# Performance work log

Measured on AMD Instinct MI355X. Metric: run time of the kernel, lower is better.

The kernel has to match this reference:

```python
import jax, jax.numpy as jnp
import numpy as np

K_TOP = 2
N_HEADS = 4

def _ln(x, g, b, eps=1e-5):
    mu = x.mean(-1, keepdims=True)
    var = ((x - mu) ** 2).mean(-1, keepdims=True)
    return (x - mu) * jax.lax.rsqrt(var + eps) * g + b

def setup_inputs() -> dict:
    key = jax.random.key(0)
    ks = jax.random.split(key, 12)
    B, Na, dz, da = 1024, 32, 96, 32
    D = dz + da
    E, F, Hh, nr = 8, 1024, 512, 4
    s = 0.02
    rn = lambda k, sh: jax.random.normal(k, sh, jnp.float32) * s
    return dict(
        z=jax.random.normal(ks[0], (B, Na, dz), jnp.float32),
        a=jax.random.normal(ks[1], (B, Na, da), jnp.float32),
        w_gate=rn(ks[2], (Na * D, E)),
        w_in=rn(ks[3], (E, 3 * D, D)), b_in=jnp.zeros((E, 3 * D), jnp.float32),
        w_out=rn(ks[4], (E, D, D)), b_out=jnp.zeros((E, D), jnp.float32),
        ln1_g=jnp.ones((E, D), jnp.float32), ln1_b=jnp.zeros((E, D), jnp.float32),
        w1=rn(ks[5], (E, F, D)), b1=jnp.zeros((E, F), jnp.float32),
        w2=rn(ks[6], (E, D, F)), b2=jnp.zeros((E, D), jnp.float32),
        ln2_g=jnp.ones((E, D), jnp.float32), ln2_b=jnp.zeros((E, D), jnp.float32),
        head_w1=rn(ks[7], (Hh, Na * D)), head_b1=jnp.zeros((Hh,), jnp.float32),
        head_w2=rn(ks[8], (nr, Hh)), head_b2=jnp.zeros((nr,), jnp.float32),
    )

def reference(z, a, w_gate, w_in, b_in, w_out, b_out, ln1_g, ln1_b, w1, b1, w2, b2, ln2_g, ln2_b, head_w1, head_b1, head_w2, head_b2):
    B, Na, _ = z.shape
    x = jnp.concatenate([z, a], axis=-1)          # [B, Na, D]
    D = x.shape[-1]
    E = w_gate.shape[1]
    hd = D // N_HEADS
    x_flat = x.reshape(B, -1)                     # [B, Na*D]

    # --- NoisyTopKRouter (eval: clean logits only) ---
    logits = x_flat @ w_gate                      # [B, E]
    top_vals, top_idx = jax.lax.top_k(logits, min(K_TOP + 1, E))
    tk_gates = jax.nn.softmax(top_vals[:, :K_TOP], axis=1)
    gates = jnp.zeros_like(logits).at[jnp.arange(B)[:, None], top_idx[:, :K_TOP]].set(tk_gates)
    load = (gates > 0).sum(0).astype(jnp.float32)
    importance = gates.sum(0)
    cv2 = lambda v: jnp.var(v, ddof=1) / (jnp.mean(v) ** 2 + 1e-10)
    loss_bal = cv2(importance) + cv2(load) + jax.scipy.special.logsumexp(logits, axis=-1).mean()

    # --- expert (self-attn + FFN, pre/post-LN residual) ---
    def expert(p):
        wi, bi, wo, bo, g1, be1, W1, B1, W2, B2, g2, be2 = p
        qkv = x @ wi.T + bi                       # [B, Na, 3D]
        q, k_, v = jnp.split(qkv, 3, axis=-1)
        q = q.reshape(B, Na, N_HEADS, hd)
        k_ = k_.reshape(B, Na, N_HEADS, hd)
        v = v.reshape(B, Na, N_HEADS, hd)
        sc = jnp.einsum('bqhd,bkhd->bhqk', q, k_) / jnp.sqrt(jnp.float32(hd))
        att = jax.nn.softmax(sc, axis=-1)
        o = jnp.einsum('bhqk,bkhd->bqhd', att, v).reshape(B, Na, D)
        o = o @ wo.T + bo
        h = _ln(x + o, g1, be1)
        f = jax.nn.relu(h @ W1.T + B1) @ W2.T + B2
        return _ln(h + f, g2, be2)

    def body(y, p):
        *ep, gate_e = p                           # gate_e: [B]
        y = y + gate_e[:, None, None] * expert(tuple(ep))
        return y, None

    xs = (w_in, b_in, w_out, b_out, ln1_g, ln1_b, w1, b1, w2, b2, ln2_g, ln2_b, gates.T)
    y, _ = jax.lax.scan(body, jnp.zeros_like(x), xs)

    y_flat = y.reshape(B, -1)
    r = jax.nn.relu(y_flat @ head_w1.T + head_b1) @ head_w2.T + head_b2  # [B, n_r]
    return r, gates, loss_bal
```

## Files before the change

kernel.cpp:

```cpp
#include <hip/hip_runtime.h>
#include <math.h>


typedef short bf16x8 __attribute__((ext_vector_type(8)));
typedef float f32x4 __attribute__((ext_vector_type(4)));
typedef unsigned short u16;

#define MFMA(a, b, c) __builtin_amdgcn_mfma_f32_16x16x32_bf16((a), (b), (c), 0, 0, 0)

__device__ __forceinline__ u16 f2bf(float f) {
    unsigned int u = __float_as_uint(f);
    unsigned int r = u + 0x7FFFu + ((u >> 16) & 1u);
    return (u16)(r >> 16);
}
__device__ __forceinline__ float bf2f(u16 s) {
    return __uint_as_float(((unsigned int)s) << 16);
}

__global__ __launch_bounds__(256) void convert_kernel(
    const float* __restrict__ wi, const float* __restrict__ wo,
    const float* __restrict__ w1, const float* __restrict__ w2,
    const float* __restrict__ hw1,
    u16* __restrict__ wiB, u16* __restrict__ woB, u16* __restrict__ w1B,
    u16* __restrict__ w2B, u16* __restrict__ hw1B)
{
    int i4 = blockIdx.x * 256 + threadIdx.x;
    int e = i4 * 4;
    const float* s; u16* d; int off;
    if (e < 393216)       { s = wi;  d = wiB;  off = e; }
    else if (e < 524288)  { s = wo;  d = woB;  off = e - 393216; }
    else if (e < 1572864) { s = w1;  d = w1B;  off = e - 524288; }
    else if (e < 2621440) { s = w2;  d = w2B;  off = e - 1572864; }
    else                  { s = hw1; d = hw1B; off = e - 2621440; }
    float4 v = *(const float4*)(s + off);
    ushort4 o;
    o.x = f2bf(v.x); o.y = f2bf(v.y); o.z = f2bf(v.z); o.w = f2bf(v.w);
    *(ushort4*)(d + off) = o;
}

__global__ __launch_bounds__(256) void router_kernel(
    const float* __restrict__ z, const float* __restrict__ a,
    const float* __restrict__ wg,
    float* __restrict__ gates_out, float* __restrict__ lse_ws,
    int* __restrict__ topi, float* __restrict__ topg)
{
    __shared__ float red[256][9];
    const int b = blockIdx.x, t = threadIdx.x;
    float acc[8];
#pragma unroll
    for (int e = 0; e < 8; ++e) acc[e] = 0.f;
#pragma unroll
    for (int i = 0; i < 16; ++i) {
        int f = i * 256 + t;
        int n = f >> 7, d = f & 127;
        float xv = (d < 96) ? z[(b * 32 + n) * 96 + d]
                            : a[(b * 32 + n) * 32 + d - 96];
        const float* wr = wg + f * 8;
#pragma unroll
        for (int e = 0; e < 8; ++e) acc[e] += xv * wr[e];
    }
#pragma unroll
    for (int e = 0; e < 8; ++e) red[t][e] = acc[e];
    __syncthreads();
    for (int s = 128; s; s >>= 1) {
        if (t < s) {
#pragma unroll
            for (int e = 0; e < 8; ++e) red[t][e] += red[t + s][e];
        }
        __syncthreads();
    }
    if (t == 0) {
        float L[8];
#pragma unroll
        for (int e = 0; e < 8; ++e) L[e] = red[0][e];
        int i0 = 0;
#pragma unroll
        for (int e = 1; e < 8; ++e) if (L[e] > L[i0]) i0 = e;
        int i1 = -1; float v1 = -3.0e38f;
#pragma unroll
        for (int e = 0; e < 8; ++e) if (e != i0 && L[e] > v1) { v1 = L[e]; i1 = e; }
        float e1 = expf(v1 - L[i0]);
        float inv = 1.f / (1.f + e1);
        float g0 = inv, g1 = e1 * inv;
#pragma unroll
        for (int e = 0; e < 8; ++e)
            gates_out[b * 8 + e] = (e == i0) ? g0 : ((e == i1) ? g1 : 0.f);
        float m = L[i0];
        float se = 0.f;
#pragma unroll
        for (int e = 0; e < 8; ++e) se += expf(L[e] - m);
        lse_ws[b] = m + logf(se);
        topi[b * 2 + 0] = i0; topi[b * 2 + 1] = i1;
        topg[b * 2 + 0] = g0; topg[b * 2 + 1] = g1;
    }
}

__global__ __launch_bounds__(1024) void build_loss_kernel(
    const int* __restrict__ topi, const float* __restrict__ topg,
    const float* __restrict__ lse,
    int* __restrict__ cnts, int* __restrict__ ent, float* __restrict__ out_loss)
{
    __shared__ int sc_[8];
    __shared__ float red[9][1024];
    const int t = threadIdx.x;
    if (t < 8) sc_[t] = 0;
    __syncthreads();
    int e0 = topi[t * 2], e1 = topi[t * 2 + 1];
    float g0 = topg[t * 2], g1 = topg[t * 2 + 1];
    int p0 = atomicAdd(&sc_[e0], 1);
    ent[e0 * 2048 + p0] = t * 2;
    int p1 = atomicAdd(&sc_[e1], 1);
    ent[e1 * 2048 + p1] = t * 2 + 1;
#pragma unroll
    for (int e = 0; e < 8; ++e)
        red[e][t] = ((e == e0) ? g0 : 0.f) + ((e == e1) ? g1 : 0.f);
    red[8][t] = lse[t];
    __syncthreads();
    for (int s = 512; s; s >>= 1) {
        if (t < s) {
#pragma unroll
            for (int q = 0; q < 9; ++q) red[q][t] += red[q][t + s];
        }
        __syncthreads();
    }
    if (t == 0) {
        float cvv[2];
        for (int p = 0; p < 2; ++p) {
            float v[8], sum = 0.f;
            for (int e = 0; e < 8; ++e) {
                v[e] = p ? (float)sc_[e] : red[e][0];
                sum += v[e];
            }
            float mean = sum * (1.f / 8.f);
            float var = 0.f;
            for (int e = 0; e < 8; ++e) { float d = v[e] - mean; var += d * d; }
            var *= (1.f / 7.f);
            cvv[p] = var / (mean * mean + 1e-10f);
        }
        out_loss[0] = cvv[0] + cvv[1] + red[8][0] * (1.f / 1024.f);
    }
    __syncthreads();
    if (t < 8) cnts[t] = sc_[t];
}

#define SM_X 0
#define SM_Q 16384
#define SM_K 32768
#define SM_V 49152
#define SM_TOT 65536
#define PS_OFF 0
#define PQ_OFF 1024
#define MU_OFF 2048
#define RS_OFF 2304
#define ATTN_GRID 8192

__device__ __forceinline__ int tsw(int row, int col) {
    return row * 256 + ((col * 2) ^ ((row & 7) << 4));
}
__device__ __forceinline__ int vsw(int row, int col) {
    return row * 128 + ((col * 2) ^ ((row & 7) << 4));
}
__device__ __forceinline__ int fsw(int row, int col) {
    return row * 2048 + ((col * 2) ^ ((row & 7) << 4));
}

__global__ __launch_bounds__(512, 2) void attn_kernel(
    const float* __restrict__ z, const float* __restrict__ a,
    const u16* __restrict__ wiBF, const float* __restrict__ b_in,
    const u16* __restrict__ woBF, const float* __restrict__ b_out,
    const float* __restrict__ ln1g, const float* __restrict__ ln1b,
    const int* __restrict__ cnts, const int* __restrict__ ent,
    u16* __restrict__ h1g)
{
    const int e = blockIdx.x & 7, j = blockIdx.x >> 3;
    const int cnt = cnts[e];
    if (j * 2 >= cnt) return;
    const int base = j * 2;

    __shared__ __align__(16) char sm[SM_TOT];
    const int t = threadIdx.x;
    const int w = t >> 6, l = t & 63, l16 = l & 15, lk = l >> 4;
    const int ke = lk * 8;
    const int wr = w >> 2, wc = w & 3;
    const f32x4 zv = {0.f, 0.f, 0.f, 0.f};

    int bs[2];
#pragma unroll
    for (int i = 0; i < 2; ++i) {
        int gi = base + i;
        int idx = (gi < cnt) ? gi : (cnt - 1);
        bs[i] = ent[e * 2048 + idx];
    }

#pragma unroll
    for (int i = 0; i < 2; ++i) {
        int cid = i * 512 + t;
        int row = cid >> 4;
        int cb = (cid & 15) * 8;
        int b_ = bs[row >> 5] >> 1;
        int n = row & 31;
        float4 p0, p1;
        if (cb < 96) {
            const float* zp = z + ((size_t)b_ * 32 + n) * 96 + cb;
            p0 = *(const float4*)zp; p1 = *(const float4*)(zp + 4);
        } else {
            const float* ap = a + ((size_t)b_ * 32 + n) * 32 + (cb - 96);
            p0 = *(const float4*)ap; p1 = *(const float4*)(ap + 4);
        }
        bf16x8 pk;
        pk[0] = (short)f2bf(p0.x); pk[1] = (short)f2bf(p0.y);
        pk[2] = (short)f2bf(p0.z); pk[3] = (short)f2bf(p0.w);
        pk[4] = (short)f2bf(p1.x); pk[5] = (short)f2bf(p1.y);
        pk[6] = (short)f2bf(p1.z); pk[7] = (short)f2bf(p1.w);
        *(bf16x8*)(sm + SM_X + tsw(row, cb)) = pk;
    }
    __syncthreads();

    {
        f32x4 acc[2][6];
#pragma unroll
        for (int mt = 0; mt < 2; ++mt)
#pragma unroll
            for (int q = 0; q < 6; ++q) acc[mt][q] = zv;
#pragma unroll
        for (int ks = 0; ks < 4; ++ks) {
            bf16x8 af[2];
#pragma unroll
            for (int mt = 0; mt < 2; ++mt) {
                int R = wr * 32 + mt * 16 + l16;
                af[mt] = *(const bf16x8*)(sm + SM_X + tsw(R, ks * 32 + ke));
            }
#pragma unroll
            for (int q = 0; q < 6; ++q) {
                int jj = wc * 96 + q * 16 + l16;
                bf16x8 bb = *(const bf16x8*)(wiBF + e * 49152 + jj * 128 + ks * 32 + ke);
#pragma unroll
                for (int mt = 0; mt < 2; ++mt) acc[mt][q] = MFMA(af[mt], bb, acc[mt][q]);
            }
        }
#pragma unroll
        for (int q = 0; q < 6; ++q) {
            int C = wc * 96 + q * 16 + l16;
            float bj = b_in[e * 384 + C];
#pragma unroll
            for (int mt = 0; mt < 2; ++mt)
#pragma unroll
                for (int i = 0; i < 4; ++i) {
                    int R = wr * 32 + mt * 16 + lk * 4 + i;
                    u16 val = f2bf(acc[mt][q][i] + bj);
                    if (C < 128) {
                        *(u16*)(sm + SM_Q + tsw(R, C)) = val;
                    } else if (C < 256) {
                        *(u16*)(sm + SM_K + tsw(R, C - 128)) = val;
                    } else {
                        *(u16*)(sm + SM_V + vsw(C - 256, R)) = val;
                    }
                }
        }
    }
    __syncthreads();

    {
        const int tok = w >> 2, hb = (w & 3) * 32;
        const float scale = 0.17677669529663687f;
        bf16x8 qa[2], kf[2];
#pragma unroll
        for (int mt = 0; mt < 2; ++mt) {
            int R = tok * 32 + mt * 16 + l16;
            qa[mt] = *(const bf16x8*)(sm + SM_Q + tsw(R, hb + ke));
            kf[mt] = *(const bf16x8*)(sm + SM_K + tsw(R, hb + ke));
        }
        f32x4 sc[2][2];
        sc[0][0] = MFMA(qa[0], kf[0], zv); sc[0][1] = MFMA(qa[0], kf[1], zv);
        sc[1][0] = MFMA(qa[1], kf[0], zv); sc[1][1] = MFMA(qa[1], kf[1], zv);
#pragma unroll
        for (int mt = 0; mt < 2; ++mt)
#pragma unroll
            for (int i = 0; i < 4; ++i) {
                float v0 = sc[mt][0][i] * scale, v1 = sc[mt][1][i] * scale;
                float m = fmaxf(v0, v1);
                m = fmaxf(m, __shfl_xor(m, 1)); m = fmaxf(m, __shfl_xor(m, 2));
                m = fmaxf(m, __shfl_xor(m, 4)); m = fmaxf(m, __shfl_xor(m, 8));
                float e0 = __expf(v0 - m), e1 = __expf(v1 - m);
                float ssum = e0 + e1;
                ssum += __shfl_xor(ssum, 1); ssum += __shfl_xor(ssum, 2);
                ssum += __shfl_xor(ssum, 4); ssum += __shfl_xor(ssum, 8);
                float inv = 1.f / ssum;
                int row = mt * 16 + lk * 4 + i;
                char* pb = sm + SM_X + w * 2048 + row * 64;
                int sw = (row & 3) << 4;
                *(u16*)(pb + ((l16 * 2) ^ sw)) = f2bf(e0 * inv);
                *(u16*)(pb + (((16 + l16) * 2) ^ sw)) = f2bf(e1 * inv);
            }
        bf16x8 pa[2];
#pragma unroll
        for (int mt = 0; mt < 2; ++mt) {
            int row = mt * 16 + l16;
            pa[mt] = *(const bf16x8*)(sm + SM_X + w * 2048 + row * 64 +
                                      ((ke * 2) ^ ((row & 3) << 4)));
        }
        f32x4 o[2][2];
#pragma unroll
        for (int nt = 0; nt < 2; ++nt) {
            int rv = hb + nt * 16 + l16;
            bf16x8 vb = *(const bf16x8*)(sm + SM_V + vsw(rv, tok * 32 + ke));
            o[0][nt] = MFMA(pa[0], vb, zv);
            o[1][nt] = MFMA(pa[1], vb, zv);
        }
#pragma unroll
        for (int mt = 0; mt < 2; ++mt)
#pragma unroll
            for (int nt = 0; nt < 2; ++nt)
#pragma unroll
                for (int i = 0; i < 4; ++i) {
                    int R = tok * 32 + mt * 16 + lk * 4 + i;
                    int C = hb + nt * 16 + l16;
                    *(u16*)(sm + SM_Q + tsw(R, C)) = f2bf(o[mt][nt][i]);
                }
    }
    __syncthreads();

    {
        f32x4 pr[2][2];
        pr[0][0] = zv; pr[0][1] = zv; pr[1][0] = zv; pr[1][1] = zv;
#pragma unroll
        for (int ks = 0; ks < 4; ++ks) {
            bf16x8 af[2];
#pragma unroll
            for (int mt = 0; mt < 2; ++mt) {
                int R = wr * 32 + mt * 16 + l16;
                af[mt] = *(const bf16x8*)(sm + SM_Q + tsw(R, ks * 32 + ke));
            }
#pragma unroll
            for (int nt = 0; nt < 2; ++nt) {
                int jj = wc * 32 + nt * 16 + l16;
                bf16x8 bb = *(const bf16x8*)(woBF + e * 16384 + jj * 128 + ks * 32 + ke);
                pr[0][nt] = MFMA(af[0], bb, pr[0][nt]);
                pr[1][nt] = MFMA(af[1], bb, pr[1][nt]);
            }
        }
        int C0 = wc * 32 + l16, C1 = C0 + 16;
        float bo0 = b_out[e * 128 + C0];
        float bo1 = b_out[e * 128 + C1];
        int b_ = bs[wr] >> 1;
#pragma unroll
        for (int mt = 0; mt < 2; ++mt)
#pragma unroll
            for (int i = 0; i < 4; ++i) {
                int R = wr * 32 + mt * 16 + lk * 4 + i;
                int n = R & 31;
                float x0 = (C0 < 96) ? z[((size_t)b_ * 32 + n) * 96 + C0]
                                     : a[((size_t)b_ * 32 + n) * 32 + C0 - 96];
                float x1 = (C1 < 96) ? z[((size_t)b_ * 32 + n) * 96 + C1]
                                     : a[((size_t)b_ * 32 + n) * 32 + C1 - 96];
                float u0 = pr[mt][0][i] + bo0 + x0;
                float u1v = pr[mt][1][i] + bo1 + x1;
                *(u16*)(sm + SM_K + tsw(R, C0)) = f2bf(u0);
                *(u16*)(sm + SM_K + tsw(R, C1)) = f2bf(u1v);
                float s = u0 + u1v;
                float q = u0 * u0 + u1v * u1v;
                s += __shfl_xor(s, 1); q += __shfl_xor(q, 1);
                s += __shfl_xor(s, 2); q += __shfl_xor(q, 2);
                s += __shfl_xor(s, 4); q += __shfl_xor(q, 4);
                s += __shfl_xor(s, 8); q += __shfl_xor(q, 8);
                if (l16 == 0) {
                    *(float*)(sm + SM_X + PS_OFF + (R * 4 + wc) * 4) = s;
                    *(float*)(sm + SM_X + PQ_OFF + (R * 4 + wc) * 4) = q;
                }
            }
    }
    __syncthreads();
    if (t < 64) {
        float s = 0.f, q = 0.f;
#pragma unroll
        for (int c = 0; c < 4; ++c) {
            s += *(const float*)(sm + SM_X + PS_OFF + (t * 4 + c) * 4);
            q += *(const float*)(sm + SM_X + PQ_OFF + (t * 4 + c) * 4);
        }
        float mu = s * (1.f / 128.f);
        float var = q * (1.f / 128.f) - mu * mu;
        *(float*)(sm + SM_X + MU_OFF + t * 4) = mu;
        *(float*)(sm + SM_X + RS_OFF + t * 4) = rsqrtf(var + 1e-5f);
    }
    __syncthreads();
    {
        int r_ = t >> 3, c0 = (t & 7) * 16;
        float mu_ = *(const float*)(sm + SM_X + MU_OFF + r_ * 4);
        float rs_ = *(const float*)(sm + SM_X + RS_OFF + r_ * 4);
#pragma unroll
        for (int j4 = 0; j4 < 2; ++j4) {
            int cb = c0 + j4 * 8;
            bf16x8* p = (bf16x8*)(sm + SM_K + tsw(r_, cb));
            bf16x8 vch = *p;
#pragma unroll
            for (int jj = 0; jj < 8; ++jj) {
                int c = cb + jj;
                float f = (bf2f((u16)vch[jj]) - mu_) * rs_ * ln1g[e * 128 + c] + ln1b[e * 128 + c];
                vch[jj] = (short)f2bf(f);
            }
            *p = vch;
        }
    }
    __syncthreads();
#pragma unroll
    for (int i = 0; i < 2; ++i) {
        int cid = i * 512 + t;
        int r_ = cid >> 4, cb = (cid & 15) * 8;
        int code = bs[r_ >> 5];
        u16* dst = h1g + (size_t)code * 4096 + (r_ & 31) * 128 + cb;
        *(bf16x8*)dst = *(const bf16x8*)(sm + SM_K + tsw(r_, cb));
    }
}

#define FH 0
#define FFB 16384
#define FPS 147456
#define FPQ 148480
#define FMU 149504
#define FRS 149760
#define F_TOT 150016
#define FFN_GRID 8192

__global__ __launch_bounds__(512, 2) void ffn_kernel(
    const u16* __restrict__ h1g,
    const u16* __restrict__ w1BF, const float* __restrict__ b1,
    const u16* __restrict__ w2BF, const float* __restrict__ b2,
    const float* __restrict__ ln2g, const float* __restrict__ ln2b,
    const float* __restrict__ topg, const int* __restrict__ cnts,
    const int* __restrict__ ent,
    u16* __restrict__ ybf)
{
    const int e = blockIdx.x & 7, jt = blockIdx.x >> 3;
    const int cnt = cnts[e];
    if (jt * 2 >= cnt) return;
    const int base = jt * 2;

    __shared__ __align__(16) char sm[F_TOT];
    const int t = threadIdx.x;
    const int w = t >> 6, l = t & 63, l16 = l & 15, lk = l >> 4;
    const int ke = lk * 8;
    const int wr = w >> 2, wc = w & 3;
    const f32x4 zv = {0.f, 0.f, 0.f, 0.f};

    int code2[2]; float gg2[2];
#pragma unroll
    for (int i = 0; i < 2; ++i) {
        int gi = base + i;
        int idx = (gi < cnt) ? gi : (cnt - 1);
        code2[i] = ent[e * 2048 + idx];
        gg2[i] = topg[code2[i]];
    }

#pragma unroll
    for (int it = 0; it < 2; ++it) {
        int cid = it * 512 + t;
        int row = cid >> 4, cb = (cid & 15) * 8;
        int code = code2[row >> 5];
        *(bf16x8*)(sm + FH + tsw(row, cb)) =
            *(const bf16x8*)(h1g + (size_t)code * 4096 + (row & 31) * 128 + cb);
    }
    __syncthreads();

    for (int h = 0; h < 4; ++h) {
        f32x4 acc[4][2];
#pragma unroll
        for (int mf = 0; mf < 4; ++mf) { acc[mf][0] = zv; acc[mf][1] = zv; }
#pragma unroll
        for (int ks = 0; ks < 4; ++ks) {
            bf16x8 af[4];
#pragma unroll
            for (int mf = 0; mf < 4; ++mf) {
                int R = mf * 16 + l16;
                af[mf] = *(const bf16x8*)(sm + FH + tsw(R, ks * 32 + ke));
            }
#pragma unroll
            for (int nf = 0; nf < 2; ++nf) {
                int jj = w * 128 + h * 32 + nf * 16 + l16;
                bf16x8 bb = *(const bf16x8*)(w1BF + e * 131072 + jj * 128 + ks * 32 + ke);
#pragma unroll
                for (int mf = 0; mf < 4; ++mf) acc[mf][nf] = MFMA(af[mf], bb, acc[mf][nf]);
            }
        }
#pragma unroll
        for (int nf = 0; nf < 2; ++nf) {
            int C = w * 128 + h * 32 + nf * 16 + l16;
            float bv = b1[e * 1024 + C];
#pragma unroll
            for (int mf = 0; mf < 4; ++mf)
#pragma unroll
                for (int i = 0; i < 4; ++i) {
                    int R = mf * 16 + lk * 4 + i;
                    *(u16*)(sm + FFB + fsw(R, C)) = f2bf(fmaxf(acc[mf][nf][i] + bv, 0.f));
                }
        }
    }
    __syncthreads();

    f32x4 cacc[2][2];
    cacc[0][0] = zv; cacc[0][1] = zv; cacc[1][0] = zv; cacc[1][1] = zv;
    for (int ks = 0; ks < 32; ++ks) {
        bf16x8 af[2];
#pragma unroll
        for (int mt = 0; mt < 2; ++mt) {
            int R = wr * 32 + mt * 16 + l16;
            af[mt] = *(const bf16x8*)(sm + FFB + fsw(R, ks * 32 + ke));
        }
#pragma unroll
        for (int nf = 0; nf < 2; ++nf) {
            int jj = wc * 32 + nf * 16 + l16;
            bf16x8 bb = *(const bf16x8*)(w2BF + e * 131072 + jj * 1024 + ks * 32 + ke);
            cacc[0][nf] = MFMA(af[0], bb, cacc[0][nf]);
            cacc[1][nf] = MFMA(af[1], bb, cacc[1][nf]);
        }
    }
    __syncthreads();

    {
        int C0 = wc * 32 + l16, C1 = C0 + 16;
        float b20 = b2[e * 128 + C0];
        float b21 = b2[e * 128 + C1];
#pragma unroll
        for (int mt = 0; mt < 2; ++mt)
#pragma unroll
            for (int i = 0; i < 4; ++i) {
                int R = wr * 32 + mt * 16 + lk * 4 + i;
                float h0 = bf2f(*(const u16*)(sm + FH + tsw(R, C0)));
                float h1v = bf2f(*(const u16*)(sm + FH + tsw(R, C1)));
                float u0 = cacc[mt][0][i] + b20 + h0;
                float u1v = cacc[mt][1][i] + b21 + h1v;
                *(u16*)(sm + FFB + tsw(R, C0)) = f2bf(u0);
                *(u16*)(sm + FFB + tsw(R, C1)) = f2bf(u1v);
                float s = u0 + u1v;
                float q = u0 * u0 + u1v * u1v;
                s += __shfl_xor(s, 1); q += __shfl_xor(q, 1);
                s += __shfl_xor(s, 2); q += __shfl_xor(q, 2);
                s += __shfl_xor(s, 4); q += __shfl_xor(q, 4);
                s += __shfl_xor(s, 8); q += __shfl_xor(q, 8);
                if (l16 == 0) {
                    *(float*)(sm + FPS + (R * 4 + wc) * 4) = s;
                    *(float*)(sm + FPQ + (R * 4 + wc) * 4) = q;
                }
            }
    }
    __syncthreads();
    if (t < 64) {
        float s = 0.f, q = 0.f;
#pragma unroll
        for (int c = 0; c < 4; ++c) {
            s += *(const float*)(sm + FPS + (t * 4 + c) * 4);
            q += *(const float*)(sm + FPQ + (t * 4 + c) * 4);
        }
        float mu = s * (1.f / 128.f);
        float var = q * (1.f / 128.f) - mu * mu;
        *(float*)(sm + FMU + t * 4) = mu;
        *(float*)(sm + FRS + t * 4) = rsqrtf(var + 1e-5f);
    }
    __syncthreads();
#pragma unroll
    for (int it = 0; it < 2; ++it) {
        int cid = it * 512 + t;
        int row = cid >> 4, cb = (cid & 15) * 8;
        float mu = *(const float*)(sm + FMU + row * 4);
        float rs = *(const float*)(sm + FRS + row * 4);
        int ei = row >> 5;
        float gm = gg2[ei];
        int code = code2[ei];
        int tok = code >> 1, slot = code & 1;
        bf16x8 v = *(const bf16x8*)(sm + FFB + tsw(row, cb));
        bf16x8 o;
#pragma unroll
        for (int jj = 0; jj < 8; ++jj) {
            int cc = cb + jj;
            float f = (bf2f((u16)v[jj]) - mu) * rs * ln2g[e * 128 + cc] + ln2b[e * 128 + cc];
            o[jj] = (short)f2bf(gm * f);
        }
        *(bf16x8*)(ybf + (size_t)(slot * 1024 + tok) * 4096 + (row & 31) * 128 + cb) = o;
    }
}

__global__ __launch_bounds__(256) void combine_kernel(
    u16* __restrict__ y0, const u16* __restrict__ y1)
{
    int i = (blockIdx.x * 256 + threadIdx.x) * 8;
    bf16x8 a = *(const bf16x8*)(y0 + i);
    bf16x8 b = *(const bf16x8*)(y1 + i);
    bf16x8 o;
#pragma unroll
    for (int j = 0; j < 8; ++j)
        o[j] = (short)f2bf(bf2f((u16)a[j]) + bf2f((u16)b[j]));
    *(bf16x8*)(y0 + i) = o;
}

__global__ __launch_bounds__(256) void head1_mfma(
    const u16* __restrict__ y_bf, const u16* __restrict__ hw1BF,
    const float* __restrict__ hb1, float* __restrict__ h_act)
{
    const int t = threadIdx.x, w = t >> 6, l = t & 63, l16 = l & 15, lk = l >> 4;
    const int ke = lk * 8;
    const int mb = blockIdx.x * 32, cb = blockIdx.y * 64 + w * 16;
    const f32x4 zv = {0.f, 0.f, 0.f, 0.f};
    f32x4 acc[2]; acc[0] = zv; acc[1] = zv;
    const u16* arow0 = y_bf + (size_t)(mb + l16) * 4096;
    const u16* arow1 = y_bf + (size_t)(mb + 16 + l16) * 4096;
    const u16* brow  = hw1BF + (size_t)(cb + l16) * 4096;
    for (int k0 = 0; k0 < 4096; k0 += 32) {
        bf16x8 a0 = *(const bf16x8*)(arow0 + k0 + ke);
        bf16x8 a1 = *(const bf16x8*)(arow1 + k0 + ke);
        bf16x8 bb = *(const bf16x8*)(brow + k0 + ke);
        acc[0] = MFMA(a0, bb, acc[0]);
        acc[1] = MFMA(a1, bb, acc[1]);
    }
    int col = cb + l16;
    float bv = hb1[col];
#pragma unroll
    for (int mt = 0; mt < 2; ++mt)
#pragma unroll
        for (int i = 0; i < 4; ++i) {
            int row = mb + mt * 16 + lk * 4 + i;
            h_act[(size_t)row * 512 + col] = fmaxf(acc[mt][i] + bv, 0.f);
        }
}

__global__ __launch_bounds__(64) void head2_kernel(
    const float* __restrict__ h_act, const float* __restrict__ w2,
    const float* __restrict__ b2, float* __restrict__ r)
{
    const int b = blockIdx.x, t = threadIdx.x;
    float a0 = 0.f, a1 = 0.f, a2 = 0.f, a3 = 0.f;
    for (int h = t; h < 512; h += 64) {
        float hv = h_act[b * 512 + h];
        a0 += hv * w2[h];
        a1 += hv * w2[512 + h];
        a2 += hv * w2[1024 + h];
        a3 += hv * w2[1536 + h];
    }
#pragma unroll
    for (int off = 32; off; off >>= 1) {
        a0 += __shfl_down(a0, off);
        a1 += __shfl_down(a1, off);
        a2 += __shfl_down(a2, off);
        a3 += __shfl_down(a3, off);
    }
    if (t == 0) {
        r[b * 4 + 0] = a0 + b2[0];
        r[b * 4 + 1] = a1 + b2[1];
        r[b * 4 + 2] = a2 + b2[2];
        r[b * 4 + 3] = a3 + b2[3];
    }
}

extern "C" void kernel_launch(void* const* d_in, const int* in_sizes, int n_in,
                              void* d_out, int out_size, void* d_ws, size_t ws_size,
                              hipStream_t stream) {
    const float* z    = (const float*)d_in[0];
    const float* a    = (const float*)d_in[1];
    const float* wg   = (const float*)d_in[2];
    const float* w_in = (const float*)d_in[3];
    const float* b_in = (const float*)d_in[4];
    const float* w_o  = (const float*)d_in[5];
    const float* b_o  = (const float*)d_in[6];
    const float* l1g  = (const float*)d_in[7];
    const float* l1b  = (const float*)d_in[8];
    const float* w1   = (const float*)d_in[9];
    const float* b1   = (const float*)d_in[10];
    const float* w2   = (const float*)d_in[11];
    const float* b2   = (const float*)d_in[12];
    const float* l2g  = (const float*)d_in[13];
    const float* l2b  = (const float*)d_in[14];
    const float* hw1  = (const float*)d_in[15];
    const float* hb1  = (const float*)d_in[16];
    const float* hw2  = (const float*)d_in[17];
    const float* hb2  = (const float*)d_in[18];

    float* out = (float*)d_out;
    float* r_out     = out;
    float* gates_out = out + 4096;
    float* loss_out  = out + 12288;

    char* W = (char*)d_ws;
    u16*   wiBF  = (u16*)(W + 0);
    u16*   woBF  = (u16*)(W + 786432);
    u16*   w1BF  = (u16*)(W + 1048576);
    u16*   w2BF  = (u16*)(W + 3145728);
    u16*   hw1BF = (u16*)(W + 5242880);
    u16*   ybf   = (u16*)(W + 9437184);
    u16*   h1g   = (u16*)(W + 26214400);
    float* h_act = (float*)(W + 42991616);
    float* lse   = (float*)(W + 45088768);
    float* topg  = (float*)(W + 45092864);
    int*   topi  = (int*)  (W + 45101056);
    int*   cnts  = (int*)  (W + 45109248);
    int*   ent   = (int*)  (W + 45109376);

    convert_kernel<<<4608, 256, 0, stream>>>(w_in, w_o, w1, w2, hw1,
                                             wiBF, woBF, w1BF, w2BF, hw1BF);
    router_kernel<<<1024, 256, 0, stream>>>(z, a, wg, gates_out, lse, topi, topg);
    build_loss_kernel<<<1, 1024, 0, stream>>>(topi, topg, lse, cnts, ent, loss_out);
    attn_kernel<<<ATTN_GRID, 512, 0, stream>>>(z, a, wiBF, b_in, woBF, b_o,
        l1g, l1b, cnts, ent, h1g);
    ffn_kernel<<<FFN_GRID, 512, 0, stream>>>(h1g, w1BF, b1, w2BF, b2,
        l2g, l2b, topg, cnts, ent, ybf);
    combine_kernel<<<2048, 256, 0, stream>>>(ybf, ybf + 4194304);
    head1_mfma<<<dim3(32, 8), 256, 0, stream>>>(ybf, hw1BF, hb1, h_act);
    head2_kernel<<<1024, 64, 0, stream>>>(h_act, hw2, hb2, r_out);
}
```

Baseline: 322.9 us.

## Register-prefetch FFN weights and fold slot combine into head1 GEMM

```diff
diff --git a/kernel.cpp b/kernel.cpp
--- a/kernel.cpp
+++ b/kernel.cpp
@@ -421,7 +421,7 @@
 #define F_TOT 150016
 #define FFN_GRID 8192
 
-__global__ __launch_bounds__(512, 2) void ffn_kernel(
+__global__ __launch_bounds__(512, 1) void ffn_kernel(
     const u16* __restrict__ h1g,
     const u16* __restrict__ w1BF, const float* __restrict__ b1,
     const u16* __restrict__ w2BF, const float* __restrict__ b2,
@@ -461,56 +461,93 @@
     }
     __syncthreads();
 
-    for (int h = 0; h < 4; ++h) {
-        f32x4 acc[4][2];
-#pragma unroll
-        for (int mf = 0; mf < 4; ++mf) { acc[mf][0] = zv; acc[mf][1] = zv; }
-#pragma unroll
-        for (int ks = 0; ks < 4; ++ks) {
-            bf16x8 af[4];
-#pragma unroll
-            for (int mf = 0; mf < 4; ++mf) {
-                int R = mf * 16 + l16;
-                af[mf] = *(const bf16x8*)(sm + FH + tsw(R, ks * 32 + ke));
+    {
+        const u16* w1b = w1BF + e * 131072;
+        bf16x8 wbuf[2][2][4];
+#pragma unroll
+        for (int nf = 0; nf < 2; ++nf)
+#pragma unroll
+            for (int ks = 0; ks < 4; ++ks)
+                wbuf[0][nf][ks] = *(const bf16x8*)(
+                    w1b + (size_t)(w * 128 + nf * 16 + l16) * 128 + ks * 32 + ke);
+#pragma unroll
+        for (int h = 0; h < 4; ++h) {
+            const int cb_ = h & 1, nb_ = cb_ ^ 1;
+            if (h < 3) {
+#pragma unroll
+                for (int nf = 0; nf < 2; ++nf)
+#pragma unroll
+                    for (int ks = 0; ks < 4; ++ks)
+                        wbuf[nb_][nf][ks] = *(const bf16x8*)(
+                            w1b + (size_t)(w * 128 + (h + 1) * 32 + nf * 16 + l16) * 128 +
+                            ks * 32 + ke);
+            }
+            f32x4 acc[4][2];
+#pragma unroll
+            for (int mf = 0; mf < 4; ++mf) { acc[mf][0] = zv; acc[mf][1] = zv; }
+#pragma unroll
+            for (int ks = 0; ks < 4; ++ks) {
+                bf16x8 af[4];
+#pragma unroll
+                for (int mf = 0; mf < 4; ++mf) {
+                    int R = mf * 16 + l16;
+                    af[mf] = *(const bf16x8*)(sm + FH + tsw(R, ks * 32 + ke));
+                }
+#pragma unroll
+                for (int nf = 0; nf < 2; ++nf)
+#pragma unroll
+                    for (int mf = 0; mf < 4; ++mf)
+                        acc[mf][nf] = MFMA(af[mf], wbuf[cb_][nf][ks], acc[mf][nf]);
             }
 #pragma unroll
             for (int nf = 0; nf < 2; ++nf) {
-                int jj = w * 128 + h * 32 + nf * 16 + l16;
-                bf16x8 bb = *(const bf16x8*)(w1BF + e * 131072 + jj * 128 + ks * 32 + ke);
-#pragma unroll
-                for (int mf = 0; mf < 4; ++mf) acc[mf][nf] = MFMA(af[mf], bb, acc[mf][nf]);
-            }
-        }
-#pragma unroll
-        for (int nf = 0; nf < 2; ++nf) {
-            int C = w * 128 + h * 32 + nf * 16 + l16;
-            float bv = b1[e * 1024 + C];
-#pragma unroll
-            for (int mf = 0; mf < 4; ++mf)
-#pragma unroll
-                for (int i = 0; i < 4; ++i) {
-                    int R = mf * 16 + lk * 4 + i;
-                    *(u16*)(sm + FFB + fsw(R, C)) = f2bf(fmaxf(acc[mf][nf][i] + bv, 0.f));
-                }
+                int C = w * 128 + h * 32 + nf * 16 + l16;
+                float bv = b1[e * 1024 + C];
+#pragma unroll
+                for (int mf = 0; mf < 4; ++mf)
+#pragma unroll
+                    for (int i = 0; i < 4; ++i) {
+                        int R = mf * 16 + lk * 4 + i;
+                        *(u16*)(sm + FFB + fsw(R, C)) =
+                            f2bf(fmaxf(acc[mf][nf][i] + bv, 0.f));
+                    }
+            }
         }
     }
     __syncthreads();
 
     f32x4 cacc[2][2];
     cacc[0][0] = zv; cacc[0][1] = zv; cacc[1][0] = zv; cacc[1][1] = zv;
-    for (int ks = 0; ks < 32; ++ks) {
-        bf16x8 af[2];
-#pragma unroll
-        for (int mt = 0; mt < 2; ++mt) {
-            int R = wr * 32 + mt * 16 + l16;
-            af[mt] = *(const bf16x8*)(sm + FFB + fsw(R, ks * 32 + ke));
-        }
-#pragma unroll
-        for (int nf = 0; nf < 2; ++nf) {
-            int jj = wc * 32 + nf * 16 + l16;
-            bf16x8 bb = *(const bf16x8*)(w2BF + e * 131072 + jj * 1024 + ks * 32 + ke);
-            cacc[0][nf] = MFMA(af[0], bb, cacc[0][nf]);
-            cacc[1][nf] = MFMA(af[1], bb, cacc[1][nf]);
+    {
+        const u16* w2p0 = w2BF + e * 131072 + (size_t)(wc * 32 + l16) * 1024;
+        const u16* w2p1 = w2p0 + 16 * 1024;
+        bf16x8 w2b[2][2][8];
+#pragma unroll
+        for (int k = 0; k < 8; ++k) {
+            w2b[0][0][k] = *(const bf16x8*)(w2p0 + k * 32 + ke);
+            w2b[0][1][k] = *(const bf16x8*)(w2p1 + k * 32 + ke);
+        }
+#pragma unroll
+        for (int g = 0; g < 4; ++g) {
+            const int cb_ = g & 1, nb_ = cb_ ^ 1;
+            if (g < 3) {
+#pragma unroll
+                for (int k = 0; k < 8; ++k) {
+                    int ks = (g + 1) * 8 + k;
+                    w2b[nb_][0][k] = *(const bf16x8*)(w2p0 + ks * 32 + ke);
+                    w2b[nb_][1][k] = *(const bf16x8*)(w2p1 + ks * 32 + ke);
+                }
+            }
+#pragma unroll
+            for (int k = 0; k < 8; ++k) {
+                int ks = g * 8 + k;
+                bf16x8 af0 = *(const bf16x8*)(sm + FFB + fsw(wr * 32 + l16, ks * 32 + ke));
+                bf16x8 af1 = *(const bf16x8*)(sm + FFB + fsw(wr * 32 + 16 + l16, ks * 32 + ke));
+                cacc[0][0] = MFMA(af0, w2b[cb_][0][k], cacc[0][0]);
+                cacc[0][1] = MFMA(af0, w2b[cb_][1][k], cacc[0][1]);
+                cacc[1][0] = MFMA(af1, w2b[cb_][0][k], cacc[1][0]);
+                cacc[1][1] = MFMA(af1, w2b[cb_][1][k], cacc[1][1]);
+            }
         }
     }
     __syncthreads();
@@ -578,19 +615,6 @@
     }
 }
 
-__global__ __launch_bounds__(256) void combine_kernel(
-    u16* __restrict__ y0, const u16* __restrict__ y1)
-{
-    int i = (blockIdx.x * 256 + threadIdx.x) * 8;
-    bf16x8 a = *(const bf16x8*)(y0 + i);
-    bf16x8 b = *(const bf16x8*)(y1 + i);
-    bf16x8 o;
-#pragma unroll
-    for (int j = 0; j < 8; ++j)
-        o[j] = (short)f2bf(bf2f((u16)a[j]) + bf2f((u16)b[j]));
-    *(bf16x8*)(y0 + i) = o;
-}
-
 __global__ __launch_bounds__(256) void head1_mfma(
     const u16* __restrict__ y_bf, const u16* __restrict__ hw1BF,
     const float* __restrict__ hb1, float* __restrict__ h_act)
@@ -600,15 +624,22 @@
     const int mb = blockIdx.x * 32, cb = blockIdx.y * 64 + w * 16;
     const f32x4 zv = {0.f, 0.f, 0.f, 0.f};
     f32x4 acc[2]; acc[0] = zv; acc[1] = zv;
-    const u16* arow0 = y_bf + (size_t)(mb + l16) * 4096;
-    const u16* arow1 = y_bf + (size_t)(mb + 16 + l16) * 4096;
-    const u16* brow  = hw1BF + (size_t)(cb + l16) * 4096;
+    const u16* s0r0 = y_bf + (size_t)(mb + l16) * 4096;
+    const u16* s0r1 = y_bf + (size_t)(mb + 16 + l16) * 4096;
+    const u16* s1r0 = s0r0 + 4194304;
+    const u16* s1r1 = s0r1 + 4194304;
+    const u16* brow = hw1BF + (size_t)(cb + l16) * 4096;
+#pragma unroll 2
     for (int k0 = 0; k0 < 4096; k0 += 32) {
-        bf16x8 a0 = *(const bf16x8*)(arow0 + k0 + ke);
-        bf16x8 a1 = *(const bf16x8*)(arow1 + k0 + ke);
         bf16x8 bb = *(const bf16x8*)(brow + k0 + ke);
+        bf16x8 a0 = *(const bf16x8*)(s0r0 + k0 + ke);
+        bf16x8 a1 = *(const bf16x8*)(s0r1 + k0 + ke);
+        bf16x8 c0 = *(const bf16x8*)(s1r0 + k0 + ke);
+        bf16x8 c1 = *(const bf16x8*)(s1r1 + k0 + ke);
         acc[0] = MFMA(a0, bb, acc[0]);
         acc[1] = MFMA(a1, bb, acc[1]);
+        acc[0] = MFMA(c0, bb, acc[0]);
+        acc[1] = MFMA(c1, bb, acc[1]);
     }
     int col = cb + l16;
     float bv = hb1[col];
@@ -700,7 +731,6 @@
         l1g, l1b, cnts, ent, h1g);
     ffn_kernel<<<FFN_GRID, 512, 0, stream>>>(h1g, w1BF, b1, w2BF, b2,
         l2g, l2b, topg, cnts, ent, ybf);
-    combine_kernel<<<2048, 256, 0, stream>>>(ybf, ybf + 4194304);
     head1_mfma<<<dim3(32, 8), 256, 0, stream>>>(ybf, hw1BF, hb1, h_act);
     head2_kernel<<<1024, 64, 0, stream>>>(h_act, hw2, hb2, r_out);
 }
```

Measured after the change: 344.5 us. 6.7% more time.
